# Kernel optimization log

Hardware: AMD Instinct MI355X
Metric: run time of the kernel (lower is better)

## Reference

```python
import jax, jax.numpy as jnp
import numpy as np

N_NODES = 100000
N_EDGES = 1000000
IN_DIM = 128
HID = 128
OUT_DIM = 40


def setup_inputs() -> dict:
    key = jax.random.key(0)
    ks = jax.random.split(key, 16)
    x = jax.random.normal(ks[0], (N_NODES, IN_DIM), dtype=jnp.float32)
    edge_index = jax.random.randint(ks[1], (2, N_EDGES), 0, N_NODES, dtype=jnp.int64)
    s = 0.05
    # GAT layer 1 (in->hid, heads=1, concat=True)
    W1 = jax.random.normal(ks[2], (HID, IN_DIM), jnp.float32) * s
    b1 = jnp.zeros((HID,), jnp.float32)
    att1 = jax.random.normal(ks[3], (1, 2 * HID), jnp.float32) * s
    bias1 = jnp.zeros((HID,), jnp.float32)
    # GAT layer 2 (hid->hid)
    W2 = jax.random.normal(ks[4], (HID, HID), jnp.float32) * s
    b2 = jnp.zeros((HID,), jnp.float32)
    att2 = jax.random.normal(ks[5], (1, 2 * HID), jnp.float32) * s
    bias2 = jnp.zeros((HID,), jnp.float32)
    # post_mp: Linear(hid,hid) -> Dropout -> Linear(hid,out)
    Wp1 = jax.random.normal(ks[6], (HID, HID), jnp.float32) * s
    bp1 = jnp.zeros((HID,), jnp.float32)
    Wp2 = jax.random.normal(ks[7], (OUT_DIM, HID), jnp.float32) * s
    bp2 = jnp.zeros((OUT_DIM,), jnp.float32)
    return dict(x=x, edge_index=edge_index, W1=W1, b1=b1, att1=att1, bias1=bias1,
                W2=W2, b2=b2, att2=att2, bias2=bias2,
                Wp1=Wp1, bp1=bp1, Wp2=Wp2, bp2=bp2)


def gat_layer(x, src, dst, W, b, att, bias, n_nodes):
    # x: [N, Fin] -> h: [N, C] (heads=1, concat=True)
    h = x @ W.T + b
    C = h.shape[1]
    att_i, att_j = att[0, :C], att[0, C:]  # split: first half pairs with x_i (dst), second with x_j (src)
    # per-node scalar projections, then gather per edge (avoids [E,2C] concat)
    e = (h @ att_i)[dst] + (h @ att_j)[src]  # [E]
    e = jnp.where(e > 0, e, 0.2 * e)  # leaky_relu(0.2)
    # segment softmax over destination nodes
    m = jax.ops.segment_max(e, dst, num_segments=n_nodes)
    ex = jnp.exp(e - m[dst])
    denom = jax.ops.segment_sum(ex, dst, num_segments=n_nodes)
    alpha = ex / denom[dst]
    out = jax.ops.segment_sum(h[src] * alpha[:, None], dst, num_segments=n_nodes)
    return out + bias


def reference(x, edge_index, W1, b1, att1, bias1, W2, b2, att2, bias2, Wp1, bp1, Wp2, bp2):
    src, dst = edge_index[0], edge_index[1]
    n = x.shape[0]
    h = jax.nn.relu(gat_layer(x, src, dst, W1, b1, att1, bias1, n))  # dropout p=0 -> identity
    h = jax.nn.relu(gat_layer(h, src, dst, W2, b2, att2, bias2, n))
    y = (h @ Wp1.T + bp1) @ Wp2.T + bp2  # post_mp (eval: dropout identity)
    return jax.nn.log_softmax(y, axis=1)
```

## Files before the change

kernel.cpp:

```cpp
#include <hip/hip_runtime.h>

#define N_NODES 100000
#define N_EDGES 1000000
#define HID 128
#define OUT_DIM 40
#define CSR_W 64
#define CUR_STRIDE 16
#define GEMM_TILES 1563
#define EDGE_BLK 977
#define WC_BLK 21

typedef __attribute__((ext_vector_type(8))) short bf16x8;
typedef __attribute__((ext_vector_type(4))) float f32x4;
typedef unsigned short ushort_t;

__device__ inline unsigned short f2bf(float f) {
    unsigned u = __float_as_uint(f);
    u += 0x7fffu + ((u >> 16) & 1u);
    return (unsigned short)(u >> 16);
}
__device__ inline float bf2f(unsigned short u) {
    return __uint_as_float(((unsigned)u) << 16);
}

__device__ inline float4 ld4(const float* p) { return *(const float4*)p; }
__device__ inline float4 ld4(const unsigned short* p) {
    ushort4 u = *(const ushort4*)p;
    return make_float4(bf2f(u.x), bf2f(u.y), bf2f(u.z), bf2f(u.w));
}

__global__ __launch_bounds__(256) void zero_kernel(float4* __restrict__ p, int n4) {
    int i = blockIdx.x * 256 + threadIdx.x;
    int stride = gridDim.x * 256;
    float4 z = make_float4(0.f, 0.f, 0.f, 0.f);
    for (; i < n4; i += stride) p[i] = z;
}

#define LDA 136
template<typename AT>
__device__ __forceinline__ void gemm_tile_body(
    int tile, const AT* __restrict__ A, const float* __restrict__ W,
    const float* __restrict__ out_bias, const float* __restrict__ in_bias,
    int relu_in, const float* __restrict__ att,
    unsigned short* __restrict__ Cb, float* __restrict__ hi, float* __restrict__ hj,
    int n_rows, unsigned short* As, unsigned short* Ws)
{
    const int t = threadIdx.x;
    const int row0 = tile * 64;

    for (int i = 0; i < 8; i++) {
        int lin = t + i * 256;
        int r = lin >> 5;
        int k = (lin & 31) * 4;
        int gr = row0 + r;
        float4 av = make_float4(0.f, 0.f, 0.f, 0.f);
        if (gr < n_rows) av = ld4(A + (size_t)gr * HID + k);
        if (in_bias) {
            av.x += in_bias[k + 0]; av.y += in_bias[k + 1];
            av.z += in_bias[k + 2]; av.w += in_bias[k + 3];
            if (relu_in) {
                av.x = fmaxf(av.x, 0.f); av.y = fmaxf(av.y, 0.f);
                av.z = fmaxf(av.z, 0.f); av.w = fmaxf(av.w, 0.f);
            }
        }
        ushort4 bv;
        bv.x = f2bf(av.x); bv.y = f2bf(av.y); bv.z = f2bf(av.z); bv.w = f2bf(av.w);
        *(ushort4*)(&As[r * LDA + k]) = bv;
    }
    for (int i = 0; i < 16; i++) {
        int lin = t + i * 256;
        int r = lin >> 5;
        int k = (lin & 31) * 4;
        float4 wv = *(const float4*)(W + (size_t)r * HID + k);
        ushort4 bv;
        bv.x = f2bf(wv.x); bv.y = f2bf(wv.y); bv.z = f2bf(wv.z); bv.w = f2bf(wv.w);
        *(ushort4*)(&Ws[r * LDA + k]) = bv;
    }
    __syncthreads();

    const int wave = t >> 6, lane = t & 63;
    const int lrow = lane & 15, quad = lane >> 4;
    const int wrow = wave * 16;

    f32x4 acc[8];
    #pragma unroll
    for (int ni = 0; ni < 8; ni++) acc[ni] = (f32x4){0.f, 0.f, 0.f, 0.f};

    #pragma unroll
    for (int ks = 0; ks < 4; ks++) {
        const int kb = ks * 32 + quad * 8;
        bf16x8 af = *(bf16x8*)(&As[(wrow + lrow) * LDA + kb]);
        #pragma unroll
        for (int ni = 0; ni < 8; ni++) {
            bf16x8 bfr = *(bf16x8*)(&Ws[(ni * 16 + lrow) * LDA + kb]);
            acc[ni] = __builtin_amdgcn_mfma_f32_16x16x32_bf16(af, bfr, acc[ni], 0, 0, 0);
        }
    }

    float pi[4] = {0.f, 0.f, 0.f, 0.f}, pj[4] = {0.f, 0.f, 0.f, 0.f};
    const int rbase = row0 + wrow + quad * 4;
    #pragma unroll
    for (int ni = 0; ni < 8; ni++) {
        const int col = ni * 16 + lrow;
        const float bo = out_bias[col];
        const float ai = att[col], aj = att[HID + col];
        #pragma unroll
        for (int r = 0; r < 4; r++) {
            float v = acc[ni][r] + bo;
            int gr = rbase + r;
            if (gr < n_rows) Cb[(size_t)gr * HID + col] = f2bf(v);
            pi[r] = fmaf(v, ai, pi[r]);
            pj[r] = fmaf(v, aj, pj[r]);
        }
    }
    #pragma unroll
    for (int o = 1; o < 16; o <<= 1) {
        #pragma unroll
        for (int r = 0; r < 4; r++) {
            pi[r] += __shfl_xor(pi[r], o);
            pj[r] += __shfl_xor(pj[r], o);
        }
    }
    if (lrow == 0) {
        #pragma unroll
        for (int r = 0; r < 4; r++) {
            int gr = rbase + r;
            if (gr < n_rows) { hi[gr] = pi[r]; hj[gr] = pj[r]; }
        }
    }
}

__global__ __launch_bounds__(256) void combined_prep(
    const float* __restrict__ x, const float* __restrict__ W1,
    const float* __restrict__ b1, const float* __restrict__ att1,
    const float* __restrict__ Wp1, const float* __restrict__ bp1,
    const float* __restrict__ Wp2, const float* __restrict__ bp2,
    const int* __restrict__ src, const int* __restrict__ dst,
    unsigned* __restrict__ cursor, int* __restrict__ csr,
    unsigned short* __restrict__ hbuf, float* __restrict__ hi, float* __restrict__ hj,
    float* __restrict__ Wc, float* __restrict__ bc)
{
    __shared__ unsigned short As[64 * LDA];
    __shared__ unsigned short Ws[128 * LDA];
    const int b = blockIdx.x, g = b >> 3, r = b & 7;

    if (r < 3) {
        const int eid = g * 3 + r;
        if (eid >= EDGE_BLK) return;
        int e = eid * 1024 + threadIdx.x;
        #pragma unroll
        for (int j = 0; j < 4; j++, e += 256) {
            if (e < N_EDGES) {
                int d = dst[e], s = src[e];
                unsigned p = atomicAdd(&cursor[d << 4], 1u);
                if (p < CSR_W) __builtin_nontemporal_store(s, &csr[(d << 6) + p]);
            }
        }
        return;
    }
    const int oid = g * 5 + (r - 3);
    if (oid < WC_BLK) {
        int t = oid * 256 + threadIdx.x;
        if (t < OUT_DIM * HID) {
            int o = t >> 7, k = t & 127;
            float s = 0.f;
            for (int j = 0; j < HID; j++) s = fmaf(Wp2[o * HID + j], Wp1[j * HID + k], s);
            Wc[t] = s;
        } else if (t < OUT_DIM * HID + OUT_DIM) {
            int o = t - OUT_DIM * HID;
            float s = bp2[o];
            for (int j = 0; j < HID; j++) s = fmaf(Wp2[o * HID + j], bp1[j], s);
            bc[o] = s;
        }
        return;
    }
    const int tile = oid - WC_BLK;
    if (tile >= GEMM_TILES) return;
    gemm_tile_body<float>(tile, x, W1, b1, nullptr, 0, att1, hbuf, hi, hj, N_NODES, As, Ws);
}

__global__ __launch_bounds__(256) void gemm_mfma_b(
    const unsigned short* __restrict__ A, const float* __restrict__ W,
    const float* __restrict__ out_bias, const float* __restrict__ in_bias,
    const float* __restrict__ att,
    unsigned short* __restrict__ Cb, float* __restrict__ hi, float* __restrict__ hj,
    int n_rows)
{
    __shared__ unsigned short As[64 * LDA];
    __shared__ unsigned short Ws[128 * LDA];
    gemm_tile_body<unsigned short>(blockIdx.x, A, W, out_bias, in_bias, 1, att,
                                   Cb, hi, hj, n_rows, As, Ws);
}

__global__ __launch_bounds__(256) void fused_gat(
    const unsigned* __restrict__ cursor, const int* __restrict__ csr,
    const unsigned short* __restrict__ hb,
    const float* __restrict__ hi, const float* __restrict__ hj,
    unsigned short* __restrict__ out)
{
    const int wave = threadIdx.x >> 6;
    const int lane = threadIdx.x & 63;
    const int d = blockIdx.x * 4 + wave;
    if (d >= N_NODES) return;
    const int half = lane >> 5, hl = lane & 31;
    unsigned deg = cursor[d << 4];
    if (deg > CSR_W) deg = CSR_W;
    const int cnt = (int)deg;
    const float hid = hi[d];
    const int base = d << 6;

    int sv = 0;
    float ev = -INFINITY;
    if (lane < cnt) {
        sv = csr[base + lane];
        float e = hid + hj[sv];
        ev = e > 0.f ? e : 0.2f * e;
    }
    float m = ev;
    #pragma unroll
    for (int o = 32; o; o >>= 1) m = fmaxf(m, __shfl_xor(m, o));
    const float exv = (lane < cnt) ? __expf(ev - m) : 0.f;
    float denom = exv;
    #pragma unroll
    for (int o = 32; o; o >>= 1) denom += __shfl_xor(denom, o);

    float acc0 = 0.f, acc1 = 0.f, acc2 = 0.f, acc3 = 0.f;
    const int rowoff = hl * 4;
    for (int i = 0; i < cnt; i += 8) {
        const int e0 = i + half, e1 = e0 + 2, e2 = e0 + 4, e3 = e0 + 6;
        const int s0 = __shfl(sv, e0), s1 = __shfl(sv, e1);
        const int s2 = __shfl(sv, e2), s3 = __shfl(sv, e3);
        const float w0 = __shfl(exv, e0), w1 = __shfl(exv, e1);
        const float w2 = __shfl(exv, e2), w3 = __shfl(exv, e3);
        const ushort4 h0 = *(const ushort4*)(hb + (size_t)s0 * HID + rowoff);
        const ushort4 h1 = *(const ushort4*)(hb + (size_t)s1 * HID + rowoff);
        const ushort4 h2 = *(const ushort4*)(hb + (size_t)s2 * HID + rowoff);
        const ushort4 h3 = *(const ushort4*)(hb + (size_t)s3 * HID + rowoff);
        acc0 = fmaf(w0, bf2f(h0.x), acc0); acc1 = fmaf(w0, bf2f(h0.y), acc1);
        acc2 = fmaf(w0, bf2f(h0.z), acc2); acc3 = fmaf(w0, bf2f(h0.w), acc3);
        acc0 = fmaf(w1, bf2f(h1.x), acc0); acc1 = fmaf(w1, bf2f(h1.y), acc1);
        acc2 = fmaf(w1, bf2f(h1.z), acc2); acc3 = fmaf(w1, bf2f(h1.w), acc3);
        acc0 = fmaf(w2, bf2f(h2.x), acc0); acc1 = fmaf(w2, bf2f(h2.y), acc1);
        acc2 = fmaf(w2, bf2f(h2.z), acc2); acc3 = fmaf(w2, bf2f(h2.w), acc3);
        acc0 = fmaf(w3, bf2f(h3.x), acc0); acc1 = fmaf(w3, bf2f(h3.y), acc1);
        acc2 = fmaf(w3, bf2f(h3.z), acc2); acc3 = fmaf(w3, bf2f(h3.w), acc3);
    }
    acc0 += __shfl_xor(acc0, 32); acc1 += __shfl_xor(acc1, 32);
    acc2 += __shfl_xor(acc2, 32); acc3 += __shfl_xor(acc3, 32);

    if (half == 0) {
        const float inv = cnt ? 1.f / denom : 0.f;
        ushort4 o4;
        o4.x = f2bf(acc0 * inv); o4.y = f2bf(acc1 * inv);
        o4.z = f2bf(acc2 * inv); o4.w = f2bf(acc3 * inv);
        *(ushort4*)(out + (size_t)d * HID + rowoff) = o4;
    }
}

#define FS 132
__global__ __launch_bounds__(256) void final_proj(
    const unsigned short* __restrict__ agg, const float* __restrict__ bias2,
    const float* __restrict__ Wc, const float* __restrict__ bc,
    float* __restrict__ out)
{
    __shared__ float As[32 * FS];
    __shared__ float Wcs[OUT_DIM * FS];
    const int t = threadIdx.x;
    const int node0 = blockIdx.x * 32;
    for (int i = 0; i < 5; i++) {
        int lin = t + i * 256;
        int r = lin >> 5;
        int c4 = lin & 31;
        float4 v = *(const float4*)(Wc + r * HID + c4 * 4);
        int lo = r * FS + c4 * 4;
        Wcs[lo + 0] = v.x; Wcs[lo + 1] = v.y; Wcs[lo + 2] = v.z; Wcs[lo + 3] = v.w;
    }
    for (int i = 0; i < 4; i++) {
        int lin = t + i * 256;
        int r = lin >> 5;
        int c4 = lin & 31;
        int node = node0 + r;
        int k = c4 * 4;
        float4 v = make_float4(0.f, 0.f, 0.f, 0.f);
        if (node < N_NODES) v = ld4(agg + (size_t)node * HID + k);
        v.x = fmaxf(v.x + bias2[k + 0], 0.f);
        v.y = fmaxf(v.y + bias2[k + 1], 0.f);
        v.z = fmaxf(v.z + bias2[k + 2], 0.f);
        v.w = fmaxf(v.w + bias2[k + 3], 0.f);
        int lo = r * FS + k;
        As[lo + 0] = v.x; As[lo + 1] = v.y; As[lo + 2] = v.z; As[lo + 3] = v.w;
    }
    __syncthreads();
    const int g = t & 7;
    const int local = t >> 3;
    const int node = node0 + local;
    float acc[5];
    #pragma unroll
    for (int j = 0; j < 5; j++) acc[j] = bc[g * 5 + j];
    for (int k = 0; k < HID; k++) {
        float a = As[local * FS + k];
        #pragma unroll
        for (int j = 0; j < 5; j++)
            acc[j] = fmaf(a, Wcs[(g * 5 + j) * FS + k], acc[j]);
    }
    float mx = acc[0];
    #pragma unroll
    for (int j = 1; j < 5; j++) mx = fmaxf(mx, acc[j]);
    #pragma unroll
    for (int o = 1; o < 8; o <<= 1) mx = fmaxf(mx, __shfl_xor(mx, o));
    float s = 0.f;
    #pragma unroll
    for (int j = 0; j < 5; j++) s += expf(acc[j] - mx);
    #pragma unroll
    for (int o = 1; o < 8; o <<= 1) s += __shfl_xor(s, o);
    float lse = mx + logf(s);
    if (node < N_NODES) {
        #pragma unroll
        for (int j = 0; j < 5; j++)
            out[(size_t)node * OUT_DIM + g * 5 + j] = acc[j] - lse;
    }
}

extern "C" void kernel_launch(void* const* d_in, const int* in_sizes, int n_in,
                              void* d_out, int out_size, void* d_ws, size_t ws_size,
                              hipStream_t stream)
{
    const float* x     = (const float*)d_in[0];
    const int*   ei    = (const int*)d_in[1];
    const float* W1    = (const float*)d_in[2];
    const float* b1    = (const float*)d_in[3];
    const float* att1  = (const float*)d_in[4];
    const float* bias1 = (const float*)d_in[5];
    const float* W2    = (const float*)d_in[6];
    const float* b2    = (const float*)d_in[7];
    const float* att2  = (const float*)d_in[8];
    const float* bias2 = (const float*)d_in[9];
    const float* Wp1   = (const float*)d_in[10];
    const float* bp1   = (const float*)d_in[11];
    const float* Wp2   = (const float*)d_in[12];
    const float* bp2   = (const float*)d_in[13];
    float* out = (float*)d_out;

    const int* src = ei;
    const int* dst = ei + N_EDGES;

    char* ws = (char*)d_ws;
    unsigned short* hbuf = (unsigned short*)ws;
    unsigned short* aggb = hbuf + (size_t)N_NODES * HID;
    float* hi      = (float*)(aggb + (size_t)N_NODES * HID);
    float* hj      = hi + N_NODES;
    unsigned* cursor = (unsigned*)(hj + N_NODES);
    int* csr       = (int*)(cursor + (size_t)N_NODES * CUR_STRIDE);
    float* Wc      = (float*)(csr + (size_t)N_NODES * CSR_W);
    float* bc      = Wc + OUT_DIM * HID;

    const int prep_blocks = ((EDGE_BLK + 2) / 3) * 8;

    zero_kernel<<<512, 256, 0, stream>>>((float4*)cursor, N_NODES * CUR_STRIDE / 4);

    combined_prep<<<prep_blocks, 256, 0, stream>>>(
        x, W1, b1, att1, Wp1, bp1, Wp2, bp2, src, dst,
        cursor, csr, hbuf, hi, hj, Wc, bc);

    fused_gat<<<N_NODES / 4, 256, 0, stream>>>(cursor, csr, hbuf, hi, hj, aggb);

    gemm_mfma_b<<<GEMM_TILES, 256, 0, stream>>>(aggb, W2, b2, bias1, att2, hbuf, hi, hj, N_NODES);
    fused_gat<<<N_NODES / 4, 256, 0, stream>>>(cursor, csr, hbuf, hi, hj, aggb);

    final_proj<<<N_NODES / 32, 256, 0, stream>>>(aggb, bias2, Wc, bc, out);
}
```

Baseline: 316.3 us.

## Batch CSR-build atomics per thread and skip padded-edge gathers in aggregation

The CSR build part of the combined prep kernel now has each thread handle 8 edges. It loads all of them first, issues all the cursor atomics, then does the stores, so more atomics are in flight at once. The edge/GEMM block split is changed from 3:5 to 2:6 per group of 8, and the grid is resized to match. In the GAT aggregation loop, the tail iteration now skips gathers for edge slots beyond the neighbour count, avoiding wasted loads of hbuf rows with zero weight. The cost is extra branching and registers, and the block mix in the prep kernel shifts.

```diff
diff --git a/kernel.cpp b/kernel.cpp
--- a/kernel.cpp
+++ b/kernel.cpp
@@ -7,12 +7,11 @@
 #define CSR_W 64
 #define CUR_STRIDE 16
 #define GEMM_TILES 1563
-#define EDGE_BLK 977
+#define EDGE_BLK 489
 #define WC_BLK 21
 
 typedef __attribute__((ext_vector_type(8))) short bf16x8;
 typedef __attribute__((ext_vector_type(4))) float f32x4;
-typedef unsigned short ushort_t;
 
 __device__ inline unsigned short f2bf(float f) {
     unsigned u = __float_as_uint(f);
@@ -144,21 +143,29 @@
     __shared__ unsigned short Ws[128 * LDA];
     const int b = blockIdx.x, g = b >> 3, r = b & 7;
 
-    if (r < 3) {
-        const int eid = g * 3 + r;
+    if (r < 2) {
+        const int eid = g * 2 + r;
         if (eid >= EDGE_BLK) return;
-        int e = eid * 1024 + threadIdx.x;
-        #pragma unroll
-        for (int j = 0; j < 4; j++, e += 256) {
-            if (e < N_EDGES) {
-                int d = dst[e], s = src[e];
-                unsigned p = atomicAdd(&cursor[d << 4], 1u);
-                if (p < CSR_W) __builtin_nontemporal_store(s, &csr[(d << 6) + p]);
-            }
-        }
+        const int e0 = eid * 2048 + threadIdx.x;
+        int ds[8], ss[8];
+        #pragma unroll
+        for (int j = 0; j < 8; j++) {
+            int e = e0 + j * 256;
+            bool v = e < N_EDGES;
+            ds[j] = v ? dst[e] : -1;
+            ss[j] = v ? src[e] : 0;
+        }
+        unsigned ps[8];
+        #pragma unroll
+        for (int j = 0; j < 8; j++)
+            if (ds[j] >= 0) ps[j] = atomicAdd(&cursor[ds[j] << 4], 1u);
+        #pragma unroll
+        for (int j = 0; j < 8; j++)
+            if (ds[j] >= 0 && ps[j] < CSR_W)
+                __builtin_nontemporal_store(ss[j], &csr[(ds[j] << 6) + ps[j]]);
         return;
     }
-    const int oid = g * 5 + (r - 3);
+    const int oid = g * 6 + (r - 2);
     if (oid < WC_BLK) {
         int t = oid * 256 + threadIdx.x;
         if (t < OUT_DIM * HID) {
@@ -232,18 +239,36 @@
         const int s2 = __shfl(sv, e2), s3 = __shfl(sv, e3);
         const float w0 = __shfl(exv, e0), w1 = __shfl(exv, e1);
         const float w2 = __shfl(exv, e2), w3 = __shfl(exv, e3);
-        const ushort4 h0 = *(const ushort4*)(hb + (size_t)s0 * HID + rowoff);
-        const ushort4 h1 = *(const ushort4*)(hb + (size_t)s1 * HID + rowoff);
-        const ushort4 h2 = *(const ushort4*)(hb + (size_t)s2 * HID + rowoff);
-        const ushort4 h3 = *(const ushort4*)(hb + (size_t)s3 * HID + rowoff);
-        acc0 = fmaf(w0, bf2f(h0.x), acc0); acc1 = fmaf(w0, bf2f(h0.y), acc1);
-        acc2 = fmaf(w0, bf2f(h0.z), acc2); acc3 = fmaf(w0, bf2f(h0.w), acc3);
-        acc0 = fmaf(w1, bf2f(h1.x), acc0); acc1 = fmaf(w1, bf2f(h1.y), acc1);
-        acc2 = fmaf(w1, bf2f(h1.z), acc2); acc3 = fmaf(w1, bf2f(h1.w), acc3);
-        acc0 = fmaf(w2, bf2f(h2.x), acc0); acc1 = fmaf(w2, bf2f(h2.y), acc1);
-        acc2 = fmaf(w2, bf2f(h2.z), acc2); acc3 = fmaf(w2, bf2f(h2.w), acc3);
-        acc0 = fmaf(w3, bf2f(h3.x), acc0); acc1 = fmaf(w3, bf2f(h3.y), acc1);
-        acc2 = fmaf(w3, bf2f(h3.z), acc2); acc3 = fmaf(w3, bf2f(h3.w), acc3);
+        if (e3 < cnt) {
+            const ushort4 h0 = *(const ushort4*)(hb + (size_t)s0 * HID + rowoff);
+            const ushort4 h1 = *(const ushort4*)(hb + (size_t)s1 * HID + rowoff);
+            const ushort4 h2 = *(const ushort4*)(hb + (size_t)s2 * HID + rowoff);
+            const ushort4 h3 = *(const ushort4*)(hb + (size_t)s3 * HID + rowoff);
+            acc0 = fmaf(w0, bf2f(h0.x), acc0); acc1 = fmaf(w0, bf2f(h0.y), acc1);
+            acc2 = fmaf(w0, bf2f(h0.z), acc2); acc3 = fmaf(w0, bf2f(h0.w), acc3);
+            acc0 = fmaf(w1, bf2f(h1.x), acc0); acc1 = fmaf(w1, bf2f(h1.y), acc1);
+            acc2 = fmaf(w1, bf2f(h1.z), acc2); acc3 = fmaf(w1, bf2f(h1.w), acc3);
+            acc0 = fmaf(w2, bf2f(h2.x), acc0); acc1 = fmaf(w2, bf2f(h2.y), acc1);
+            acc2 = fmaf(w2, bf2f(h2.z), acc2); acc3 = fmaf(w2, bf2f(h2.w), acc3);
+            acc0 = fmaf(w3, bf2f(h3.x), acc0); acc1 = fmaf(w3, bf2f(h3.y), acc1);
+            acc2 = fmaf(w3, bf2f(h3.z), acc2); acc3 = fmaf(w3, bf2f(h3.w), acc3);
+        } else {
+            if (e0 < cnt) {
+                const ushort4 h0 = *(const ushort4*)(hb + (size_t)s0 * HID + rowoff);
+                acc0 = fmaf(w0, bf2f(h0.x), acc0); acc1 = fmaf(w0, bf2f(h0.y), acc1);
+                acc2 = fmaf(w0, bf2f(h0.z), acc2); acc3 = fmaf(w0, bf2f(h0.w), acc3);
+            }
+            if (e1 < cnt) {
+                const ushort4 h1 = *(const ushort4*)(hb + (size_t)s1 * HID + rowoff);
+                acc0 = fmaf(w1, bf2f(h1.x), acc0); acc1 = fmaf(w1, bf2f(h1.y), acc1);
+                acc2 = fmaf(w1, bf2f(h1.z), acc2); acc3 = fmaf(w1, bf2f(h1.w), acc3);
+            }
+            if (e2 < cnt) {
+                const ushort4 h2 = *(const ushort4*)(hb + (size_t)s2 * HID + rowoff);
+                acc0 = fmaf(w2, bf2f(h2.x), acc0); acc1 = fmaf(w2, bf2f(h2.y), acc1);
+                acc2 = fmaf(w2, bf2f(h2.z), acc2); acc3 = fmaf(w2, bf2f(h2.w), acc3);
+            }
+        }
     }
     acc0 += __shfl_xor(acc0, 32); acc1 += __shfl_xor(acc1, 32);
     acc2 += __shfl_xor(acc2, 32); acc3 += __shfl_xor(acc3, 32);
@@ -354,7 +379,7 @@
     float* Wc      = (float*)(csr + (size_t)N_NODES * CSR_W);
     float* bc      = Wc + OUT_DIM * HID;
 
-    const int prep_blocks = ((EDGE_BLK + 2) / 3) * 8;
+    const int prep_blocks = 264 * 8;
 
     zero_kernel<<<512, 256, 0, stream>>>((float4*)cursor, N_NODES * CUR_STRIDE / 4);
 
```

Result: slower. 346.2 us (+9.5%).
